# Optimization experiments

Hardware: AMD Instinct MI355X
Metric: run time of the kernel (lower is better)

Reference implementation:

```python
import jax, jax.numpy as jnp
import numpy as np

H = 16        # num query heads
H_KV = 4      # num kv heads
D = 128       # head_dim
ROPE_BASE = 10000.0


def rotate_half(x):
    x1, x2 = jnp.split(x, 2, axis=-1)
    return jnp.concatenate((-x2, x1), axis=-1)


def rope_tables(T, d, dtype):
    inv_freq = 1.0 / (ROPE_BASE ** (np.arange(0, d, 2, dtype=np.float32) / d))
    t = np.arange(T, dtype=np.float32)
    freqs = np.outer(t, inv_freq)                 # [T, d/2]
    emb = np.concatenate((freqs, freqs), axis=-1)  # [T, d]
    return jnp.asarray(np.cos(emb), dtype), jnp.asarray(np.sin(emb), dtype)


def setup_inputs() -> dict:
    key = jax.random.key(0)
    ks = jax.random.split(key, 5)
    B, T, C = 2, 2048, 2048
    s = 0.02
    return {
        "x": jax.random.normal(ks[0], (B, T, C), jnp.float32),
        "wq": jax.random.normal(ks[1], (C, H * D), jnp.float32) * s,
        "wk": jax.random.normal(ks[2], (C, H_KV * D), jnp.float32) * s,
        "wv": jax.random.normal(ks[3], (C, H_KV * D), jnp.float32) * s,
        "wo": jax.random.normal(ks[4], (H * D, C), jnp.float32) * s,
    }


def reference(x, wq, wk, wv, wo):
    B, T, C = x.shape
    # QKV projections (bias=False); weights stored as [in, out]
    q = (x @ wq).reshape(B, T, H, D).transpose(0, 2, 1, 3)      # [B,H,T,D]
    k = (x @ wk).reshape(B, T, H_KV, D).transpose(0, 2, 1, 3)   # [B,Hkv,T,D]
    v = (x @ wv).reshape(B, T, H_KV, D).transpose(0, 2, 1, 3)
    # RoPE
    cos, sin = rope_tables(T, D, x.dtype)                        # [T,D]
    q = q * cos + rotate_half(q) * sin
    k = k * cos + rotate_half(k) * sin
    # GQA: repeat kv heads
    n_rep = H // H_KV
    k = jnp.repeat(k, n_rep, axis=1)                             # [B,H,T,D]
    v = jnp.repeat(v, n_rep, axis=1)
    # Causal SDPA
    scale = 1.0 / jnp.sqrt(jnp.asarray(D, x.dtype))
    att = jnp.einsum('bhqd,bhkd->bhqk', q, k) * scale            # [B,H,T,T]
    causal = jnp.tril(jnp.ones((T, T), dtype=bool))
    att = jnp.where(causal, att, jnp.asarray(-jnp.inf, x.dtype))
    att = jax.nn.softmax(att, axis=-1)
    y = jnp.einsum('bhqk,bhkd->bhqd', att, v)                    # [B,H,T,D]
    y = y.transpose(0, 2, 1, 3).reshape(B, T, H * D)
    return y @ wo
```

## Files before the change

### kernel.cpp

```cpp
#include <hip/hip_runtime.h>
#include <cstdint>
#include <cstddef>

typedef __attribute__((ext_vector_type(8))) short short8;
typedef __attribute__((ext_vector_type(4))) float f4;
typedef __attribute__((ext_vector_type(4))) unsigned int u4;

static __device__ __forceinline__ unsigned short f2bf(float x) {
  unsigned int u = __float_as_uint(x);
  unsigned int r = (u + 0x7FFFu + ((u >> 16) & 1u)) >> 16;
  return (unsigned short)r;
}

static __device__ __forceinline__ void gll16(const unsigned short* g, unsigned short* l) {
  __builtin_amdgcn_global_load_lds(
      (const __attribute__((address_space(1))) unsigned int*)g,
      (__attribute__((address_space(3))) unsigned int*)l, 16, 0, 0);
}

template <int N>
static __device__ __forceinline__ void wait_vmcnt() {
  if constexpr (N == 0) asm volatile("s_waitcnt vmcnt(0)" ::: "memory");
  else if constexpr (N == 1) asm volatile("s_waitcnt vmcnt(1)" ::: "memory");
  else if constexpr (N == 2) asm volatile("s_waitcnt vmcnt(2)" ::: "memory");
  else if constexpr (N == 3) asm volatile("s_waitcnt vmcnt(3)" ::: "memory");
  else if constexpr (N == 4) asm volatile("s_waitcnt vmcnt(4)" ::: "memory");
}

__global__ __launch_bounds__(256) void k_cvt(
    const float* __restrict__ src, unsigned short* __restrict__ dst) {
  int gid = blockIdx.x * 256 + threadIdx.x;
  const float* p = src + (size_t)gid * 8;
  f4 a = *(const f4*)p;
  f4 b = *(const f4*)(p + 4);
  union { unsigned short u[8]; u4 v; } pk;
#pragma unroll
  for (int i = 0; i < 4; ++i) { pk.u[i] = f2bf(a[i]); pk.u[4 + i] = f2bf(b[i]); }
  *(u4*)(dst + (size_t)gid * 8) = pk.v;
}

__global__ __launch_bounds__(256) void k_transpose_f(
    const float* __restrict__ src, unsigned short* __restrict__ dst, int R, int C) {
  __shared__ alignas(16) unsigned short tile[64 * 72];
  int tid = threadIdx.x;
  int c0 = blockIdx.x * 64, r0 = blockIdx.y * 64;
#pragma unroll
  for (int s = 0; s < 2; ++s) {
    int chunk = tid + s * 256;
    int c8 = chunk & 7, r = chunk >> 3;
    const float* p = src + (size_t)(r0 + r) * C + c0 + c8 * 8;
    f4 a = *(const f4*)p;
    f4 b = *(const f4*)(p + 4);
    union { unsigned short u[8]; u4 v; } pk;
#pragma unroll
    for (int i = 0; i < 4; ++i) { pk.u[i] = f2bf(a[i]); pk.u[4 + i] = f2bf(b[i]); }
    *(u4*)(tile + r * 72 + c8 * 8) = pk.v;
  }
  __syncthreads();
#pragma unroll
  for (int s = 0; s < 2; ++s) {
    int chunk = tid + s * 256;
    int r8 = chunk & 7, c = chunk >> 3;
    union { unsigned short u[8]; u4 v; } pk;
#pragma unroll
    for (int i = 0; i < 8; ++i) pk.u[i] = tile[(r8 * 8 + i) * 72 + c];
    *(u4*)(dst + (size_t)(c0 + c) * R + r0 + r8 * 8) = pk.v;
  }
}

#define PHASE(QM, QN, WAITC, ...)                                              \
  {                                                                            \
    wait_vmcnt<WAITC>();                                                       \
    __builtin_amdgcn_s_barrier();                                              \
    asm volatile("" ::: "memory");                                             \
    short8 af[FI][2], bf[2][2];                                                \
    _Pragma("unroll") for (int i = 0; i < FI; ++i)                             \
      _Pragma("unroll") for (int ks = 0; ks < 2; ++ks)                         \
        af[i][ks] = *(const short8*)(&As[cur][((QM) * (BM / 2) + wm * (BM / 4) + i * 16 + l16) * 64 + kswz[ks]]); \
    _Pragma("unroll") for (int j = 0; j < 2; ++j)                              \
      _Pragma("unroll") for (int ks = 0; ks < 2; ++ks)                         \
        bf[j][ks] = *(const short8*)(&Bs[cur][((QN) * 128 + wn * 32 + j * 16 + l16) * 64 + kswz[ks]]); \
    __VA_ARGS__                                                                \
    __builtin_amdgcn_s_setprio(1);                                             \
    _Pragma("unroll") for (int i = 0; i < FI; ++i)                             \
      _Pragma("unroll") for (int j = 0; j < 2; ++j)                            \
        _Pragma("unroll") for (int ks = 0; ks < 2; ++ks)                       \
          acc[(QM) * FI + i][(QN) * 2 + j] = __builtin_amdgcn_mfma_f32_16x16x32_bf16( \
              af[i][ks], bf[j][ks], acc[(QM) * FI + i][(QN) * 2 + j], 0, 0, 0); \
    __builtin_amdgcn_s_setprio(0);                                             \
  }

template <int BM, bool BF16OUT>
__global__ __launch_bounds__(512, 2) void k_gemm8(
    const unsigned short* __restrict__ A, const unsigned short* __restrict__ Bt,
    void* __restrict__ Cout, int M, int N, int K) {
  constexpr int CA = BM / 128;
  constexpr int FI = BM / 64;
  constexpr int WA = 2 + CA, WB = 2 * CA, WC = CA + 2, PB = CA;
  __shared__ alignas(16) unsigned short As[2][BM * 64];
  __shared__ alignas(16) unsigned short Bs[2][256 * 64];
  (void)M;

  int tid = threadIdx.x;
  int wid = tid >> 6, lane = tid & 63, quad = lane >> 4, l16 = lane & 15;
  int wm = wid >> 2, wn = wid & 3;

  int nx = gridDim.x;
  int id = blockIdx.y * nx + blockIdx.x;
  int nwg = nx * gridDim.y;
  int per = nwg >> 3;
  int lin = (id & 7) * per + (id >> 3);
  int bx = lin % nx, by = lin / nx;
  int bm = by * BM, bn = bx * 256;

  int srow = lane >> 3;
  int scol = ((lane & 7) ^ srow) << 3;
  const unsigned short* Ast = A + (size_t)(bm + wid * 8 + srow) * K + scol;
  const unsigned short* Bst = Bt + (size_t)(bn + wid * 8 + srow) * K + scol;
  const int ldsw = wid * 512;

  int kswz[2];
#pragma unroll
  for (int ks = 0; ks < 2; ++ks) kswz[ks] = (ks * 32 + quad * 8) ^ ((l16 & 7) << 3);

  f4 zero = {0.f, 0.f, 0.f, 0.f};
  f4 acc[2 * FI][4];
#pragma unroll
  for (int i = 0; i < 2 * FI; ++i)
#pragma unroll
    for (int j = 0; j < 4; ++j) acc[i][j] = zero;

  if constexpr (CA == 2) {
    gll16(Ast, &As[0][ldsw]);
    gll16(Ast + (size_t)64 * K, &As[0][ldsw + 64 * 64]);
  } else {
    gll16(Ast, &As[0][ldsw]);
  }
  gll16(Bst, &Bs[0][ldsw]);
  gll16(Bst + (size_t)64 * K, &Bs[0][ldsw + 64 * 64]);
  gll16(Bst + (size_t)128 * K, &Bs[0][ldsw + 128 * 64]);
  gll16(Bst + (size_t)192 * K, &Bs[0][ldsw + 192 * 64]);
  if constexpr (CA == 2) {
    gll16(Ast + (size_t)128 * K, &As[0][ldsw + 128 * 64]);
    gll16(Ast + (size_t)192 * K, &As[0][ldsw + 192 * 64]);
  } else {
    gll16(Ast + (size_t)64 * K, &As[0][ldsw + 64 * 64]);
  }

  int nt = K >> 6;
  int cur = 0;
  for (int t = 0; t < nt - 1; ++t) {
    int k0n = (t + 1) << 6;
    int nxt = cur ^ 1;
    unsigned short* Asn = &As[nxt][0];
    unsigned short* Bsn = &Bs[nxt][0];
    PHASE(0, 0, WA,
      if constexpr (CA == 2) {
        gll16(Ast + k0n, Asn + ldsw);
        gll16(Ast + (size_t)64 * K + k0n, Asn + ldsw + 64 * 64);
      } else {
        gll16(Ast + k0n, Asn + ldsw);
      })
    PHASE(0, 1, WB,
      gll16(Bst + k0n, Bsn + ldsw);
      gll16(Bst + (size_t)64 * K + k0n, Bsn + ldsw + 64 * 64);)
    PHASE(1, 0, WC,
      gll16(Bst + (size_t)128 * K + k0n, Bsn + ldsw + 128 * 64);
      gll16(Bst + (size_t)192 * K + k0n, Bsn + ldsw + 192 * 64);)
    PHASE(1, 1, -1,
      if constexpr (CA == 2) {
        gll16(Ast + (size_t)128 * K + k0n, Asn + ldsw + 128 * 64);
        gll16(Ast + (size_t)192 * K + k0n, Asn + ldsw + 192 * 64);
      } else {
        gll16(Ast + (size_t)64 * K + k0n, Asn + ldsw + 64 * 64);
      })
    cur = nxt;
  }
  PHASE(0, 0, WA, ;)
  PHASE(0, 1, PB, ;)
  PHASE(1, 0, 0, ;)
  PHASE(1, 1, -1, ;)

#pragma unroll
  for (int mi = 0; mi < 2 * FI; ++mi) {
    int row = bm + (mi / FI) * (BM / 2) + wm * (BM / 4) + (mi % FI) * 16 + quad * 4;
#pragma unroll
    for (int nj = 0; nj < 4; ++nj) {
      int col = bn + (nj >> 1) * 128 + wn * 32 + (nj & 1) * 16 + l16;
#pragma unroll
      for (int r = 0; r < 4; ++r) {
        if constexpr (BF16OUT)
          ((unsigned short*)Cout)[(size_t)(row + r) * N + col] = f2bf(acc[mi][nj][r]);
        else
          ((float*)Cout)[(size_t)(row + r) * N + col] = acc[mi][nj][r];
      }
    }
  }
}

__global__ __launch_bounds__(256) void k_rope8(unsigned short* __restrict__ QKV) {
  int gid = blockIdx.x * 256 + threadIdx.x;
  int c8 = gid & 7; int g = gid >> 3;
  int h20 = g % 20; g /= 20;
  int t = g & 2047; int b = g >> 11;
  bool isq = h20 < 16;
  size_t p = (size_t)(b * 2048 + t) * 3072 +
             (isq ? h20 * 128 : 2048 + (h20 - 16) * 128) + c8 * 8;
  short8 x0 = *(const short8*)(QKV + p);
  short8 x1 = *(const short8*)(QKV + p + 64);
  short8 o0, o1;
  float tf = (float)t;
#pragma unroll
  for (int i = 0; i < 8; ++i) {
    int d = c8 * 8 + i;
    float a0 = __uint_as_float((unsigned int)(unsigned short)x0[i] << 16);
    float a1 = __uint_as_float((unsigned int)(unsigned short)x1[i] << 16);
    float freq = exp2f(-(float)d * 0.20762050593046f);
    float ang = tf * freq;
    float cv = __cosf(ang), sv = __sinf(ang);
    float r0 = a0 * cv - a1 * sv;
    float r1 = a1 * cv + a0 * sv;
    if (isq) { r0 *= 0.088388347648318f; r1 *= 0.088388347648318f; }
    o0[i] = (short)f2bf(r0);
    o1[i] = (short)f2bf(r1);
  }
  *(short8*)(QKV + p) = o0;
  *(short8*)(QKV + p + 64) = o1;
}

__global__ __launch_bounds__(256) void k_vtrans2(
    const unsigned short* __restrict__ QKV, unsigned short* __restrict__ VT) {
  __shared__ alignas(16) unsigned short tile[64 * 72];
  int tid = threadIdx.x;
  int t0 = blockIdx.x * 64;
  int g = blockIdx.y;
  int dh = g & 1, hk = (g >> 1) & 3, b = g >> 3;
  int d0 = dh * 64;
  const unsigned short* src = QKV + (size_t)(b * 2048 + t0) * 3072 + 2560 + hk * 128 + d0;
#pragma unroll
  for (int s = 0; s < 2; ++s) {
    int chunk = tid + s * 256;
    int c8 = chunk & 7, r = chunk >> 3;
    *(u4*)(tile + r * 72 + c8 * 8) = *(const u4*)(src + (size_t)r * 3072 + c8 * 8);
  }
  __syncthreads();
  unsigned short* dst = VT + ((size_t)((b * 4 + hk) * 128 + d0)) * 2048 + t0;
#pragma unroll
  for (int s = 0; s < 2; ++s) {
    int chunk = tid + s * 256;
    int r8 = chunk & 7, c = chunk >> 3;
    union { unsigned short u[8]; u4 v; } pk;
#pragma unroll
    for (int i = 0; i < 8; ++i) pk.u[i] = tile[(r8 * 8 + i) * 72 + c];
    *(u4*)(dst + (size_t)c * 2048 + r8 * 8) = pk.v;
  }
}

static __device__ __forceinline__ void attn_step(
    const unsigned short* __restrict__ Ks, const unsigned short* __restrict__ Vs,
    const short8* qf, f4* o, float& m, float& l,
    int quad, int l16, int qrow, int K0, bool mask, bool odd) {
  f4 zero = {0.f, 0.f, 0.f, 0.f};
  f4 st[4];
#pragma unroll
  for (int kt = 0; kt < 4; ++kt) {
    st[kt] = zero;
#pragma unroll
    for (int ks = 0; ks < 4; ++ks) {
      short8 kf = *(const short8*)(Ks + (kt * 16 + l16) * 136 + ks * 32 + quad * 8);
      st[kt] = __builtin_amdgcn_mfma_f32_16x16x32_bf16(kf, qf[ks], st[kt], 0, 0, 0);
    }
  }
  if (mask) {
#pragma unroll
    for (int kt = 0; kt < 4; ++kt)
#pragma unroll
      for (int r = 0; r < 4; ++r)
        if (K0 + kt * 16 + quad * 4 + r > qrow) st[kt][r] = -1e30f;
  }
  float sm = -1e30f;
#pragma unroll
  for (int kt = 0; kt < 4; ++kt)
#pragma unroll
    for (int r = 0; r < 4; ++r) sm = fmaxf(sm, st[kt][r]);
  sm = fmaxf(sm, __shfl_xor(sm, 16));
  sm = fmaxf(sm, __shfl_xor(sm, 32));
  bool grow = !__all(sm - m <= 8.f);
  float mnew = grow ? fmaxf(m, sm) : m;
  f4 pv[4];
  float rs = 0.f;
#pragma unroll
  for (int kt = 0; kt < 4; ++kt)
#pragma unroll
    for (int r = 0; r < 4; ++r) {
      pv[kt][r] = __expf(st[kt][r] - mnew);
      rs += pv[kt][r];
    }
  rs += __shfl_xor(rs, 16);
  rs += __shfl_xor(rs, 32);
  if (grow) {
    float alpha = __expf(m - mnew);
    l = l * alpha + rs;
    m = mnew;
#pragma unroll
    for (int i = 0; i < 8; ++i) o[i] *= alpha;
  } else {
    l += rs;
  }
  unsigned int c[4][2];
#pragma unroll
  for (int kt = 0; kt < 4; ++kt)
#pragma unroll
    for (int p = 0; p < 2; ++p)
      asm("v_cvt_pk_bf16_f32 %0, %1, %2"
          : "=v"(c[kt][p]) : "v"(pv[kt][2 * p]), "v"(pv[kt][2 * p + 1]));
#pragma unroll
  for (int kh = 0; kh < 2; ++kh) {
    unsigned int A0 = c[2 * kh][0], A1 = c[2 * kh][1];
    unsigned int B0 = c[2 * kh + 1][0], B1 = c[2 * kh + 1][1];
    asm("v_permlane32_swap_b32 %0, %1" : "+v"(A0), "+v"(B0));
    asm("v_permlane32_swap_b32 %0, %1" : "+v"(A1), "+v"(B1));
    unsigned int tA0 = (unsigned int)__builtin_amdgcn_ds_swizzle((int)A0, 0x401F);
    unsigned int tA1 = (unsigned int)__builtin_amdgcn_ds_swizzle((int)A1, 0x401F);
    unsigned int tB0 = (unsigned int)__builtin_amdgcn_ds_swizzle((int)B0, 0x401F);
    unsigned int tB1 = (unsigned int)__builtin_amdgcn_ds_swizzle((int)B1, 0x401F);
    union { unsigned int u[4]; short8 s; } pb;
    pb.u[0] = odd ? tB0 : A0;
    pb.u[1] = odd ? tB1 : A1;
    pb.u[2] = odd ? B0 : tA0;
    pb.u[3] = odd ? B1 : tA1;
#pragma unroll
    for (int i = 0; i < 8; ++i) {
      short8 vf = *(const short8*)(Vs + (i * 16 + l16) * 72 + kh * 32 + quad * 8);
      o[i] = __builtin_amdgcn_mfma_f32_16x16x32_bf16(vf, pb.s, o[i], 0, 0, 0);
    }
  }
}

__global__ __launch_bounds__(256, 2) void k_attn(
    const unsigned short* __restrict__ QKV,
    const unsigned short* __restrict__ VT,
    unsigned short* __restrict__ Y) {
  __shared__ alignas(16) unsigned short Ks[2][64 * 136];
  __shared__ alignas(16) unsigned short Vs[2][128 * 72];
  int tid = threadIdx.x;
  int w = tid >> 6, lane = tid & 63, quad = lane >> 4, l16 = lane & 15;
  bool odd = (quad & 1) != 0;
  int bh = blockIdx.y; int b = bh >> 4, h = bh & 15, hk = h >> 2;
  int v = blockIdx.x;
  int q0A = v * 64 + w * 16;
  int q0B = (31 - v) * 64 + w * 16;
  const unsigned short* Qh = QKV + (size_t)b * 2048 * 3072 + h * 128;
  const unsigned short* Kh = QKV + (size_t)b * 2048 * 3072 + 2048 + hk * 128;
  const unsigned short* Vh = VT + ((size_t)(b * 4 + hk) * 128) * 2048;

  int rK0 = tid >> 4, cK = tid & 15;
  int rV0 = tid >> 3, cV = tid & 7;

  short8 qfA[4], qfB[4];
#pragma unroll
  for (int ks = 0; ks < 4; ++ks) {
    qfA[ks] = *(const short8*)(Qh + (size_t)(q0A + l16) * 3072 + ks * 32 + quad * 8);
    qfB[ks] = *(const short8*)(Qh + (size_t)(q0B + l16) * 3072 + ks * 32 + quad * 8);
  }

  f4 zero = {0.f, 0.f, 0.f, 0.f};
  f4 oA[8], oB[8];
#pragma unroll
  for (int i = 0; i < 8; ++i) { oA[i] = zero; oB[i] = zero; }
  float mA = -1e30f, lA = 0.f, mB = -1e30f, lB = 0.f;

  int nch = 32 - v;

#pragma unroll
  for (int s = 0; s < 4; ++s) {
    int rK = rK0 + 16 * s;
    *(u4*)(&Ks[0][0] + rK * 136 + cK * 8) =
        *(const u4*)(Kh + (size_t)rK * 3072 + cK * 8);
    int rV = rV0 + 32 * s;
    *(u4*)(&Vs[0][0] + rV * 72 + cV * 8) =
        *(const u4*)(Vh + (size_t)rV * 2048 + cV * 8);
  }
  __syncthreads();

  for (int kc = 0; kc < nch; ++kc) {
    int cur = kc & 1, nxt = cur ^ 1;
    int K0 = kc * 64;
    bool have_next = (kc + 1) < nch;
    u4 kreg[4], vreg[4];
    if (have_next) {
      int K0n = K0 + 64;
#pragma unroll
      for (int s = 0; s < 4; ++s) {
        int rK = rK0 + 16 * s;
        kreg[s] = *(const u4*)(Kh + (size_t)(K0n + rK) * 3072 + cK * 8);
        int rV = rV0 + 32 * s;
        vreg[s] = *(const u4*)(Vh + (size_t)rV * 2048 + K0n + cV * 8);
      }
    }

    if (kc <= v)
      attn_step(&Ks[cur][0], &Vs[cur][0], qfA, oA, mA, lA, quad, l16, q0A + l16, K0, kc == v, odd);
    attn_step(&Ks[cur][0], &Vs[cur][0], qfB, oB, mB, lB, quad, l16, q0B + l16, K0, kc == nch - 1, odd);

    if (have_next) {
#pragma unroll
      for (int s = 0; s < 4; ++s) {
        int rK = rK0 + 16 * s;
        *(u4*)(&Ks[nxt][0] + rK * 136 + cK * 8) = kreg[s];
        int rV = rV0 + 32 * s;
        *(u4*)(&Vs[nxt][0] + rV * 72 + cV * 8) = vreg[s];
      }
    }
    __syncthreads();
  }

  float rA = 1.f / lA, rB = 1.f / lB;
  size_t yrowA = (size_t)(b * 2048 + q0A + l16) * 2048 + h * 128;
  size_t yrowB = (size_t)(b * 2048 + q0B + l16) * 2048 + h * 128;
#pragma unroll
  for (int i = 0; i < 8; ++i)
#pragma unroll
    for (int r = 0; r < 4; ++r) {
      Y[yrowA + i * 16 + quad * 4 + r] = f2bf(oA[i][r] * rA);
      Y[yrowB + i * 16 + quad * 4 + r] = f2bf(oB[i][r] * rB);
    }
}

extern "C" void kernel_launch(void* const* d_in, const int* in_sizes, int n_in,
                              void* d_out, int out_size, void* d_ws, size_t ws_size,
                              hipStream_t stream) {
  const float* x  = (const float*)d_in[0];
  const float* wq = (const float*)d_in[1];
  const float* wk = (const float*)d_in[2];
  const float* wv = (const float*)d_in[3];
  const float* wo = (const float*)d_in[4];
  float* outp = (float*)d_out;

  unsigned short* WqkvT = (unsigned short*)d_out;
  unsigned short* VT    = WqkvT + (size_t)3072 * 2048;
  unsigned short* Xb    = VT + (size_t)2 * 4 * 128 * 2048;
  unsigned short* QKV = (unsigned short*)d_ws;
  unsigned short* Yb  = QKV + (size_t)4096 * 3072;
  unsigned short* WoT = QKV;

  dim3 blk(256);
  k_cvt<<<dim3(4096), blk, 0, stream>>>(x, Xb);
  k_transpose_f<<<dim3(32, 32), blk, 0, stream>>>(wq, WqkvT, 2048, 2048);
  k_transpose_f<<<dim3(8, 32), blk, 0, stream>>>(wk, WqkvT + (size_t)2048 * 2048, 2048, 512);
  k_transpose_f<<<dim3(8, 32), blk, 0, stream>>>(wv, WqkvT + (size_t)2560 * 2048, 2048, 512);

  k_gemm8<256, true><<<dim3(12, 16), dim3(512), 0, stream>>>(
      Xb, WqkvT, QKV, 4096, 3072, 2048);

  k_rope8<<<dim3(2560), blk, 0, stream>>>(QKV);
  k_vtrans2<<<dim3(32, 16), blk, 0, stream>>>(QKV, VT);

  k_attn<<<dim3(16, 32), blk, 0, stream>>>(QKV, VT, Yb);

  k_transpose_f<<<dim3(32, 32), blk, 0, stream>>>(wo, WoT, 2048, 2048);
  k_gemm8<128, false><<<dim3(8, 32), dim3(512), 0, stream>>>(
      Yb, WoT, outp, 4096, 2048, 2048);
}
```

Measured before the change: 310.0 us.

## Widen attention blocks to 512 threads covering 128 query rows per tile pair

```diff
diff --git a/kernel.cpp b/kernel.cpp
--- a/kernel.cpp
+++ b/kernel.cpp
@@ -256,21 +256,9 @@
   }
 }
 
-static __device__ __forceinline__ void attn_step(
-    const unsigned short* __restrict__ Ks, const unsigned short* __restrict__ Vs,
-    const short8* qf, f4* o, float& m, float& l,
-    int quad, int l16, int qrow, int K0, bool mask, bool odd) {
-  f4 zero = {0.f, 0.f, 0.f, 0.f};
-  f4 st[4];
-#pragma unroll
-  for (int kt = 0; kt < 4; ++kt) {
-    st[kt] = zero;
-#pragma unroll
-    for (int ks = 0; ks < 4; ++ks) {
-      short8 kf = *(const short8*)(Ks + (kt * 16 + l16) * 136 + ks * 32 + quad * 8);
-      st[kt] = __builtin_amdgcn_mfma_f32_16x16x32_bf16(kf, qf[ks], st[kt], 0, 0, 0);
-    }
-  }
+static __device__ __forceinline__ void softmax_pack(
+    f4* st, f4* o, float& m, float& l,
+    int quad, int l16, int qrow, int K0, bool mask, bool odd, short8* pb) {
   if (mask) {
 #pragma unroll
     for (int kt = 0; kt < 4; ++kt)
@@ -324,20 +312,42 @@
     unsigned int tA1 = (unsigned int)__builtin_amdgcn_ds_swizzle((int)A1, 0x401F);
     unsigned int tB0 = (unsigned int)__builtin_amdgcn_ds_swizzle((int)B0, 0x401F);
     unsigned int tB1 = (unsigned int)__builtin_amdgcn_ds_swizzle((int)B1, 0x401F);
-    union { unsigned int u[4]; short8 s; } pb;
-    pb.u[0] = odd ? tB0 : A0;
-    pb.u[1] = odd ? tB1 : A1;
-    pb.u[2] = odd ? B0 : tA0;
-    pb.u[3] = odd ? B1 : tA1;
+    union { unsigned int u[4]; short8 s; } pk;
+    pk.u[0] = odd ? tB0 : A0;
+    pk.u[1] = odd ? tB1 : A1;
+    pk.u[2] = odd ? B0 : tA0;
+    pk.u[3] = odd ? B1 : tA1;
+    pb[kh] = pk.s;
+  }
+}
+
+static __device__ __forceinline__ void attn_single(
+    const unsigned short* __restrict__ Ks, const unsigned short* __restrict__ Vs,
+    const short8* qf, f4* o, float& m, float& l,
+    int quad, int l16, int qrow, int K0, bool mask, bool odd) {
+  f4 zero = {0.f, 0.f, 0.f, 0.f};
+  f4 st[4];
+#pragma unroll
+  for (int kt = 0; kt < 4; ++kt) {
+    st[kt] = zero;
+#pragma unroll
+    for (int ks = 0; ks < 4; ++ks) {
+      short8 kf = *(const short8*)(Ks + (kt * 16 + l16) * 136 + ks * 32 + quad * 8);
+      st[kt] = __builtin_amdgcn_mfma_f32_16x16x32_bf16(kf, qf[ks], st[kt], 0, 0, 0);
+    }
+  }
+  short8 pb[2];
+  softmax_pack(st, o, m, l, quad, l16, qrow, K0, mask, odd, pb);
+#pragma unroll
+  for (int kh = 0; kh < 2; ++kh)
 #pragma unroll
     for (int i = 0; i < 8; ++i) {
       short8 vf = *(const short8*)(Vs + (i * 16 + l16) * 72 + kh * 32 + quad * 8);
-      o[i] = __builtin_amdgcn_mfma_f32_16x16x32_bf16(vf, pb.s, o[i], 0, 0, 0);
-    }
-  }
-}
-
-__global__ __launch_bounds__(256, 2) void k_attn(
+      o[i] = __builtin_amdgcn_mfma_f32_16x16x32_bf16(vf, pb[kh], o[i], 0, 0, 0);
+    }
+}
+
+__global__ __launch_bounds__(512, 4) void k_attn(
     const unsigned short* __restrict__ QKV,
     const unsigned short* __restrict__ VT,
     unsigned short* __restrict__ Y) {
@@ -348,8 +358,8 @@
   bool odd = (quad & 1) != 0;
   int bh = blockIdx.y; int b = bh >> 4, h = bh & 15, hk = h >> 2;
   int v = blockIdx.x;
-  int q0A = v * 64 + w * 16;
-  int q0B = (31 - v) * 64 + w * 16;
+  int q0A = v * 128 + w * 16;
+  int q0B = (15 - v) * 128 + w * 16;
   const unsigned short* Qh = QKV + (size_t)b * 2048 * 3072 + h * 128;
   const unsigned short* Kh = QKV + (size_t)b * 2048 * 3072 + 2048 + hk * 128;
   const unsigned short* Vh = VT + ((size_t)(b * 4 + hk) * 128) * 2048;
@@ -370,14 +380,15 @@
   for (int i = 0; i < 8; ++i) { oA[i] = zero; oB[i] = zero; }
   float mA = -1e30f, lA = 0.f, mB = -1e30f, lB = 0.f;
 
-  int nch = 32 - v;
-
-#pragma unroll
-  for (int s = 0; s < 4; ++s) {
-    int rK = rK0 + 16 * s;
+  int nch = 32 - 2 * v;
+  int lastA = 2 * v + 1;
+
+#pragma unroll
+  for (int s = 0; s < 2; ++s) {
+    int rK = rK0 + 32 * s;
     *(u4*)(&Ks[0][0] + rK * 136 + cK * 8) =
         *(const u4*)(Kh + (size_t)rK * 3072 + cK * 8);
-    int rV = rV0 + 32 * s;
+    int rV = rV0 + 64 * s;
     *(u4*)(&Vs[0][0] + rV * 72 + cV * 8) =
         *(const u4*)(Vh + (size_t)rV * 2048 + cV * 8);
   }
@@ -387,28 +398,30 @@
     int cur = kc & 1, nxt = cur ^ 1;
     int K0 = kc * 64;
     bool have_next = (kc + 1) < nch;
-    u4 kreg[4], vreg[4];
+    u4 kreg[2], vreg[2];
     if (have_next) {
       int K0n = K0 + 64;
 #pragma unroll
-      for (int s = 0; s < 4; ++s) {
-        int rK = rK0 + 16 * s;
+      for (int s = 0; s < 2; ++s) {
+        int rK = rK0 + 32 * s;
         kreg[s] = *(const u4*)(Kh + (size_t)(K0n + rK) * 3072 + cK * 8);
-        int rV = rV0 + 32 * s;
+        int rV = rV0 + 64 * s;
         vreg[s] = *(const u4*)(Vh + (size_t)rV * 2048 + K0n + cV * 8);
       }
     }
 
-    if (kc <= v)
-      attn_step(&Ks[cur][0], &Vs[cur][0], qfA, oA, mA, lA, quad, l16, q0A + l16, K0, kc == v, odd);
-    attn_step(&Ks[cur][0], &Vs[cur][0], qfB, oB, mB, lB, quad, l16, q0B + l16, K0, kc == nch - 1, odd);
+    if (kc <= lastA)
+      attn_single(&Ks[cur][0], &Vs[cur][0], qfA, oA, mA, lA,
+                  quad, l16, q0A + l16, K0, kc >= 2 * v, odd);
+    attn_single(&Ks[cur][0], &Vs[cur][0], qfB, oB, mB, lB,
+                quad, l16, q0B + l16, K0, kc >= nch - 2, odd);
 
     if (have_next) {
 #pragma unroll
-      for (int s = 0; s < 4; ++s) {
-        int rK = rK0 + 16 * s;
+      for (int s = 0; s < 2; ++s) {
+        int rK = rK0 + 32 * s;
         *(u4*)(&Ks[nxt][0] + rK * 136 + cK * 8) = kreg[s];
-        int rV = rV0 + 32 * s;
+        int rV = rV0 + 64 * s;
         *(u4*)(&Vs[nxt][0] + rV * 72 + cV * 8) = vreg[s];
       }
     }
@@ -456,7 +469,7 @@
   k_rope8<<<dim3(2560), blk, 0, stream>>>(QKV);
   k_vtrans2<<<dim3(32, 16), blk, 0, stream>>>(QKV, VT);
 
-  k_attn<<<dim3(16, 32), blk, 0, stream>>>(QKV, VT, Yb);
+  k_attn<<<dim3(8, 32), dim3(512), 0, stream>>>(QKV, VT, Yb);
 
   k_transpose_f<<<dim3(32, 32), blk, 0, stream>>>(wo, WoT, 2048, 2048);
   k_gemm8<128, false><<<dim3(8, 32), dim3(512), 0, stream>>>(
```

New measurement: 385.1 us. 24.2% more time.
